# Optimization experiments

Measured on AMD Instinct MI355X. Metric: run time of the kernel, lower is better.

The kernel has to match this reference:

```python
import jax, jax.numpy as jnp
import numpy as np

N_NODES = 100000
N_EDGES = 1000000
DIM = 64
BN_EPS = 1e-5


def setup_inputs() -> dict:
    key = jax.random.key(0)
    k_x, k_src, k_off, k_w, k_b = jax.random.split(key, 5)
    x = jax.random.normal(k_x, (N_NODES, DIM), dtype=jnp.float32)
    # Build edges with src != dst so add_remaining_self_loops semantics reduce to
    # appending one self-loop per node (no pre-existing self loops).
    src = jax.random.randint(k_src, (N_EDGES,), 0, N_NODES, dtype=jnp.int64)
    off = jax.random.randint(k_off, (N_EDGES,), 1, N_NODES, dtype=jnp.int64)
    dst = (src + off) % N_NODES
    edge_index = jnp.stack([src, dst], axis=0)
    lin_w = jax.random.normal(k_w, (DIM, DIM), dtype=jnp.float32) * (1.0 / np.sqrt(DIM))
    lin_b = jax.random.normal(k_b, (DIM,), dtype=jnp.float32) * 0.01
    bn_gamma = jnp.ones((DIM,), dtype=jnp.float32)
    bn_beta = jnp.zeros((DIM,), dtype=jnp.float32)
    return {"x": x, "edge_index": edge_index, "lin_w": lin_w, "lin_b": lin_b,
            "bn_gamma": bn_gamma, "bn_beta": bn_beta}


def reference(x, edge_index, lin_w, lin_b, bn_gamma, bn_beta):
    N = x.shape[0]
    loops = jnp.arange(N, dtype=edge_index.dtype)
    src = jnp.concatenate([edge_index[0], loops])  # add_remaining_self_loops
    dst = jnp.concatenate([edge_index[1], loops])
    # edge_weight is rebound to None inside MySAGEConv.forward, so message == x_j
    msgs = jnp.take(x, src, axis=0)                      # [E+N, D] gather
    summed = jax.ops.segment_sum(msgs, dst, num_segments=N)
    deg = jax.ops.segment_sum(jnp.ones_like(dst, dtype=x.dtype), dst, num_segments=N)
    aggr = summed / deg[:, None]                         # scatter-mean (deg >= 1)
    out = aggr @ lin_w.T + lin_b                         # linear
    # BatchNorm1d, training mode (batch stats, biased variance)
    mean = out.mean(axis=0)
    var = out.var(axis=0)
    out = (out - mean) * jax.lax.rsqrt(var + BN_EPS) * bn_gamma + bn_beta
    out = out + x                                        # residual (in_dim == out_dim)
    return jax.nn.relu(out)
```

## Files before the change

kernel.cpp:

```cpp
#include <hip/hip_runtime.h>

#define N_NODES 100000
#define N_EDGES 1000000
#define DIM 64
#define BN_EPS 1e-5f

#define CAP 40
#define NSEG 100
#define SEG_NODES 1000
#define SEGCAP 11264
#define BCAP 64
#define EPB 3072
#define NBIN1 326
#define CONV_BLOCKS 3125
#define OVF_CAP 1024
#define GATHER_BLOCKS (N_NODES / 32)

typedef __attribute__((ext_vector_type(8))) short short8_t;
typedef __attribute__((ext_vector_type(4))) float f32x4;

__device__ inline unsigned bf16rne(float f) {
    unsigned u = __float_as_uint(f);
    return (u + 0x7FFFu + ((u >> 16) & 1u)) >> 16;
}
__device__ inline unsigned pack2(float a, float b) {
    return bf16rne(a) | (bf16rne(b) << 16);
}
__device__ inline void unp_add(unsigned d, float& e0, float& e1) {
    e0 += __uint_as_float(d << 16);
    e1 += __uint_as_float(d & 0xFFFF0000u);
}
__device__ inline void add8(float* acc, uint4 v) {
    unp_add(v.x, acc[0], acc[1]);
    unp_add(v.y, acc[2], acc[3]);
    unp_add(v.z, acc[4], acc[5]);
    unp_add(v.w, acc[6], acc[7]);
}

__global__ __launch_bounds__(256) void k_bin1(const int* __restrict__ ei,
                                              const float4* __restrict__ x4,
                                              const float* __restrict__ W,
                                              uint2* __restrict__ seg_buf,
                                              int* __restrict__ seg_cnt,
                                              int* __restrict__ ovf_cnt,
                                              uint2* __restrict__ ovf,
                                              uint4* __restrict__ xh,
                                              unsigned short* __restrict__ Wb) {
    __shared__ int cnt[NSEG];
    __shared__ int base[NSEG];
    __shared__ uint2 pairs[NSEG][BCAP];

    int b = blockIdx.x;
    if (b == NBIN1 + CONV_BLOCKS) {
        for (int t = threadIdx.x; t < DIM * DIM / 2; t += 256) {
            float2 w2 = ((const float2*)W)[t];
            ((unsigned*)Wb)[t] = pack2(w2.x, w2.y);
        }
        return;
    }
    if (b >= NBIN1) {
        int g = (b - NBIN1) * 256 + threadIdx.x;
        float4 lo = x4[2 * g];
        float4 hi = x4[2 * g + 1];
        uint4 r;
        r.x = pack2(lo.x, lo.y);
        r.y = pack2(lo.z, lo.w);
        r.z = pack2(hi.x, hi.y);
        r.w = pack2(hi.z, hi.w);
        xh[8 + g] = r;
        return;
    }

    for (int t = threadIdx.x; t < NSEG; t += 256) cnt[t] = 0;
    __syncthreads();

    const int base4 = b * (EPB / 4);
#pragma unroll
    for (int k = 0; k < 3; ++k) {
        int i4 = base4 + k * 256 + threadIdx.x;
        if (i4 < N_EDGES / 4) {
            int4 s4 = ((const int4*)ei)[i4];
            int4 d4 = ((const int4*)(ei + N_EDGES))[i4];
            int ss[4] = {s4.x, s4.y, s4.z, s4.w};
            int dd[4] = {d4.x, d4.y, d4.z, d4.w};
#pragma unroll
            for (int q = 0; q < 4; ++q) {
                int seg = (unsigned)dd[q] / SEG_NODES;
                int p = atomicAdd(&cnt[seg], 1);
                if (p < BCAP) {
                    pairs[seg][p] = make_uint2((unsigned)ss[q], (unsigned)dd[q]);
                } else {
                    int g = atomicAdd(ovf_cnt, 1);
                    if (g < OVF_CAP) ovf[g] = make_uint2((unsigned)ss[q], (unsigned)dd[q]);
                }
            }
        }
    }
    __syncthreads();

    if (threadIdx.x < NSEG) {
        int c = min(cnt[threadIdx.x], BCAP);
        base[threadIdx.x] = atomicAdd(&seg_cnt[threadIdx.x], c);
    }
    __syncthreads();

    const int wave = threadIdx.x >> 6, lane = threadIdx.x & 63;
    for (int seg = wave; seg < NSEG; seg += 4) {
        int c = min(cnt[seg], BCAP);
        int bs = base[seg];
        for (int i = lane; i < c; i += 64) {
            int pos = bs + i;
            if (pos < SEGCAP) seg_buf[seg * SEGCAP + pos] = pairs[seg][i];
        }
    }
}

__global__ __launch_bounds__(256) void k_bin2(const uint2* __restrict__ seg_buf,
                                              const int* __restrict__ seg_cnt,
                                              const int* __restrict__ ovf_cnt,
                                              const uint2* __restrict__ ovf,
                                              int* __restrict__ srcs,
                                              int* __restrict__ count) {
    const int s = blockIdx.x;
    __shared__ int lcnt[SEG_NODES];
    for (int t = threadIdx.x; t < SEG_NODES; t += 256) lcnt[t] = 0;
    __syncthreads();

    int n = seg_cnt[s];
    if (n > SEGCAP) n = SEGCAP;
    const uint2* sb = seg_buf + s * SEGCAP;

    auto place = [&](uint2 pr) {
        int dl = (int)pr.y - s * SEG_NODES;
        int p = atomicAdd(&lcnt[dl], 1);
        if (p < CAP) srcs[(int)pr.y * CAP + p] = (int)pr.x;
    };

    int i = threadIdx.x;
    for (; i + 768 < n; i += 1024) {
        uint2 a0 = sb[i];
        uint2 a1 = sb[i + 256];
        uint2 a2 = sb[i + 512];
        uint2 a3 = sb[i + 768];
        place(a0); place(a1); place(a2); place(a3);
    }
    for (; i < n; i += 256) place(sb[i]);

    int oc = *ovf_cnt;
    if (oc > OVF_CAP) oc = OVF_CAP;
    for (int t = threadIdx.x; t < oc; t += 256) {
        uint2 pr = ovf[t];
        if ((int)((unsigned)pr.y / SEG_NODES) == s) place(pr);
    }
    __syncthreads();

    for (int t = threadIdx.x; t < SEG_NODES; t += 256)
        count[s * SEG_NODES + t] = lcnt[t];
}

__global__ __launch_bounds__(256) void k_fill_legacy(const int* __restrict__ ei,
                                                     const float4* __restrict__ x4,
                                                     const float* __restrict__ W,
                                                     int* __restrict__ count,
                                                     int* __restrict__ srcs,
                                                     uint4* __restrict__ xh,
                                                     unsigned short* __restrict__ Wb) {
    int b = blockIdx.x;
    if (b == 977 + CONV_BLOCKS) {
        for (int t = threadIdx.x; t < DIM * DIM / 2; t += 256) {
            float2 w2 = ((const float2*)W)[t];
            ((unsigned*)Wb)[t] = pack2(w2.x, w2.y);
        }
        return;
    }
    if (b < 977) {
        int t = b * 256 + threadIdx.x;
        if (t < N_EDGES / 4) {
            int4 s4 = ((const int4*)ei)[t];
            int4 d4 = ((const int4*)(ei + N_EDGES))[t];
            int p0 = atomicAdd(&count[d4.x], 1);
            int p1 = atomicAdd(&count[d4.y], 1);
            int p2 = atomicAdd(&count[d4.z], 1);
            int p3 = atomicAdd(&count[d4.w], 1);
            if (p0 < CAP) srcs[d4.x * CAP + p0] = s4.x;
            if (p1 < CAP) srcs[d4.y * CAP + p1] = s4.y;
            if (p2 < CAP) srcs[d4.z * CAP + p2] = s4.z;
            if (p3 < CAP) srcs[d4.w * CAP + p3] = s4.w;
        }
    } else {
        int g = (b - 977) * 256 + threadIdx.x;
        float4 lo = x4[2 * g];
        float4 hi = x4[2 * g + 1];
        uint4 r;
        r.x = pack2(lo.x, lo.y);
        r.y = pack2(lo.z, lo.w);
        r.z = pack2(hi.x, hi.y);
        r.w = pack2(hi.z, hi.w);
        xh[8 + g] = r;
    }
}

__global__ __launch_bounds__(256) void k_gather_linear(
        const uint4* __restrict__ xh,
        const int* __restrict__ count,
        const int* __restrict__ srcs,
        const unsigned short* __restrict__ Wb,
        const float* __restrict__ bias,
        float* __restrict__ lin_out,
        float* __restrict__ stats8) {
    const int lane = threadIdx.x & 63;
    const int wave = threadIdx.x >> 6;
    const int sub  = lane >> 3;
    const int f8   = lane & 7;

    __shared__ unsigned short ab[32 * 72];
    __shared__ float red0[4][32], red1[4][32];

    const int row = blockIdx.x * 32 + wave * 8 + sub;
    float acc[8] = {0.f, 0.f, 0.f, 0.f, 0.f, 0.f, 0.f, 0.f};
    add8(acc, xh[(row + 1) * 8 + f8]);

    const int ctrue = count[row];
    const int c = (ctrue < CAP) ? ctrue : CAP;
    const int* sp = srcs + row * CAP;
    for (int i = 0; i < c; i += 4) {
        int4 e = *(const int4*)(sp + i);
        int e1 = (i + 1 < c) ? e.y : -1;
        int e2 = (i + 2 < c) ? e.z : -1;
        int e3 = (i + 3 < c) ? e.w : -1;
        uint4 v0 = xh[(e.x + 1) * 8 + f8];
        uint4 v1 = xh[(e1 + 1) * 8 + f8];
        uint4 v2 = xh[(e2 + 1) * 8 + f8];
        uint4 v3 = xh[(e3 + 1) * 8 + f8];
        add8(acc, v0);
        add8(acc, v1);
        add8(acc, v2);
        add8(acc, v3);
    }

    const float inv = 1.0f / (float)(ctrue + 1);
#pragma unroll
    for (int k = 0; k < 8; ++k) acc[k] *= inv;

    uint4 pk;
    pk.x = pack2(acc[0], acc[1]);
    pk.y = pack2(acc[2], acc[3]);
    pk.z = pack2(acc[4], acc[5]);
    pk.w = pack2(acc[6], acc[7]);
    *(uint4*)&ab[(wave * 8 + sub) * 72 + f8 * 8] = pk;
    __syncthreads();

    const int mh = wave & 1, nh = wave >> 1;
    const int m = lane & 15, quad = lane >> 4;

    const unsigned short* ap = &ab[(mh * 16 + m) * 72 + quad * 8];
    short8_t a0 = *(const short8_t*)ap;
    short8_t a1 = *(const short8_t*)(ap + 32);

    const unsigned short* bp0 = Wb + (nh * 32 + m) * 64 + quad * 8;
    short8_t b00 = *(const short8_t*)bp0;
    short8_t b01 = *(const short8_t*)(bp0 + 32);
    const unsigned short* bp1 = bp0 + 16 * 64;
    short8_t b10 = *(const short8_t*)bp1;
    short8_t b11 = *(const short8_t*)(bp1 + 32);

    f32x4 c0 = {0.f, 0.f, 0.f, 0.f}, c1 = {0.f, 0.f, 0.f, 0.f};
    c0 = __builtin_amdgcn_mfma_f32_16x16x32_bf16(a0, b00, c0, 0, 0, 0);
    c0 = __builtin_amdgcn_mfma_f32_16x16x32_bf16(a1, b01, c0, 0, 0, 0);
    c1 = __builtin_amdgcn_mfma_f32_16x16x32_bf16(a0, b10, c1, 0, 0, 0);
    c1 = __builtin_amdgcn_mfma_f32_16x16x32_bf16(a1, b11, c1, 0, 0, 0);

    const int rb = blockIdx.x * 32 + mh * 16 + quad * 4;
#pragma unroll
    for (int f = 0; f < 2; ++f) {
        f32x4 cc = f ? c1 : c0;
        int col = nh * 32 + f * 16 + m;
        float bj = bias[col];
        float q0 = 0.f, q1 = 0.f;
#pragma unroll
        for (int r = 0; r < 4; ++r) {
            float v = cc[r] + bj;
            lin_out[(rb + r) * DIM + col] = v;
            q0 += v;
            q1 += v * v;
        }
        q0 += __shfl_xor(q0, 16); q0 += __shfl_xor(q0, 32);
        q1 += __shfl_xor(q1, 16); q1 += __shfl_xor(q1, 32);
        if (quad == 0) {
            red0[wave][f * 16 + m] = q0;
            red1[wave][f * 16 + m] = q1;
        }
    }
    __syncthreads();
    if (threadIdx.x < DIM) {
        int j = threadIdx.x, jh = j >> 5, jl = j & 31;
        float t0 = red0[2 * jh][jl] + red0[2 * jh + 1][jl];
        float t1 = red1[2 * jh][jl] + red1[2 * jh + 1][jl];
        float* sb = stats8 + (blockIdx.x & 7) * 128;
        atomicAdd(&sb[j], t0);
        atomicAdd(&sb[DIM + j], t1);
    }
}

__global__ __launch_bounds__(256) void k_final(const float4* lin4,
                                               const float4* __restrict__ x4,
                                               const float* __restrict__ stats8,
                                               const float* __restrict__ gamma,
                                               const float* __restrict__ beta,
                                               float4* out4) {
    __shared__ float ss[2][DIM];
    if (threadIdx.x < DIM) {
        int j = threadIdx.x;
        float s0 = 0.f, s1 = 0.f;
#pragma unroll
        for (int b = 0; b < 8; ++b) {
            s0 += stats8[b * 128 + j];
            s1 += stats8[b * 128 + DIM + j];
        }
        const float invN = 1.0f / (float)N_NODES;
        float mean = s0 * invN;
        float var = s1 * invN - mean * mean;
        float scale = gamma[j] * rsqrtf(var + BN_EPS);
        ss[0][j] = scale;
        ss[1][j] = beta[j] - mean * scale;
    }
    __syncthreads();
    int tid = blockIdx.x * blockDim.x + threadIdx.x;
    int j4 = (tid & (DIM / 4 - 1)) * 4;
    float4 l = lin4[tid];
    float4 xv = x4[tid];
    float4 o;
    o.x = fmaxf(fmaf(l.x, ss[0][j4 + 0], ss[1][j4 + 0]) + xv.x, 0.f);
    o.y = fmaxf(fmaf(l.y, ss[0][j4 + 1], ss[1][j4 + 1]) + xv.y, 0.f);
    o.z = fmaxf(fmaf(l.z, ss[0][j4 + 2], ss[1][j4 + 2]) + xv.z, 0.f);
    o.w = fmaxf(fmaf(l.w, ss[0][j4 + 3], ss[1][j4 + 3]) + xv.w, 0.f);
    out4[tid] = o;
}

extern "C" void kernel_launch(void* const* d_in, const int* in_sizes, int n_in,
                              void* d_out, int out_size, void* d_ws, size_t ws_size,
                              hipStream_t stream) {
    const float* x     = (const float*)d_in[0];
    const int*   ei    = (const int*)d_in[1];
    const float* W     = (const float*)d_in[2];
    const float* bias  = (const float*)d_in[3];
    const float* gamma = (const float*)d_in[4];
    const float* beta  = (const float*)d_in[5];
    float* out = (float*)d_out;

    char* ws = (char*)d_ws;
    float*          stats8  = (float*)(ws);
    int*            seg_cnt = (int*)(ws + 4096);
    int*            ovf_cnt = (int*)(ws + 4608);
    uint2*          ovf     = (uint2*)(ws + 4736);
    uint4*          xh      = (uint4*)(ws + 12928);
    unsigned short* Wb      = (unsigned short*)(ws + 12813056);
    int*            count   = (int*)(ws + 12821248);
    int*            srcs    = (int*)(ws + 13221248);
    uint2*          seg_buf = (uint2*)(ws + 29221248);

    const size_t NEED_BIN = 29221248 + (size_t)NSEG * SEGCAP * 8;

    if (ws_size >= NEED_BIN) {
        hipMemsetAsync(ws, 0, 13056, stream);
        k_bin1<<<NBIN1 + CONV_BLOCKS + 1, 256, 0, stream>>>(
            ei, (const float4*)x, W, seg_buf, seg_cnt, ovf_cnt, ovf, xh, Wb);
        k_bin2<<<NSEG, 256, 0, stream>>>(seg_buf, seg_cnt, ovf_cnt, ovf,
                                         srcs, count);
    } else {
        hipMemsetAsync(ws, 0, 13056, stream);
        hipMemsetAsync(count, 0, 400000, stream);
        k_fill_legacy<<<977 + CONV_BLOCKS + 1, 256, 0, stream>>>(
            ei, (const float4*)x, W, count, srcs, xh, Wb);
    }

    k_gather_linear<<<GATHER_BLOCKS, 256, 0, stream>>>(
        xh, count, srcs, Wb, bias, out, stats8);

    k_final<<<N_NODES * (DIM / 4) / 256, 256, 0, stream>>>(
        (const float4*)out, (const float4*)x, stats8, gamma, beta, (float4*)out);
}
```

Measured before the change: 153.6 us.

## Fuse all stages into one persistent kernel with grid barriers

Replaces the separate binning, placement, gather-linear and BatchNorm-finalize kernels with a single persistent kernel. Stages are separated by software grid-wide barriers built on atomics. Linear outputs are held in registers across the BatchNorm-statistics barrier instead of being written to and re-read from global memory. The placement pass splits each segment into four sub-blocks, and the residual reads the bf16 copy of x. This aims to cut launch overhead and the global round-trip, but it relies on all blocks being co-resident for the barriers, adds register pressure, and changes the residual precision.

```diff
diff --git a/kernel.cpp b/kernel.cpp
--- a/kernel.cpp
+++ b/kernel.cpp
@@ -8,13 +8,17 @@
 #define CAP 40
 #define NSEG 100
 #define SEG_NODES 1000
-#define SEGCAP 11264
-#define BCAP 64
+#define SEGCAP 11200
+#define BCAP 48
 #define EPB 3072
 #define NBIN1 326
-#define CONV_BLOCKS 3125
-#define OVF_CAP 1024
-#define GATHER_BLOCKS (N_NODES / 32)
+#define CONV_CHUNKS 3125
+#define TOTAL_P1 (NBIN1 + CONV_CHUNKS + 1)
+#define OVF_CAP 4096
+#define SPLITB 4
+#define SEG_Q (SEG_NODES / SPLITB)
+#define NTILES (N_NODES / 32)
+#define MAXT 5
 
 typedef __attribute__((ext_vector_type(8))) short short8_t;
 typedef __attribute__((ext_vector_type(4))) float f32x4;
@@ -37,225 +41,136 @@
     unp_add(v.w, acc[6], acc[7]);
 }
 
-__global__ __launch_bounds__(256) void k_bin1(const int* __restrict__ ei,
-                                              const float4* __restrict__ x4,
-                                              const float* __restrict__ W,
-                                              uint2* __restrict__ seg_buf,
-                                              int* __restrict__ seg_cnt,
-                                              int* __restrict__ ovf_cnt,
-                                              uint2* __restrict__ ovf,
-                                              uint4* __restrict__ xh,
-                                              unsigned short* __restrict__ Wb) {
-    __shared__ int cnt[NSEG];
-    __shared__ int base[NSEG];
-    __shared__ uint2 pairs[NSEG][BCAP];
-
-    int b = blockIdx.x;
-    if (b == NBIN1 + CONV_BLOCKS) {
-        for (int t = threadIdx.x; t < DIM * DIM / 2; t += 256) {
-            float2 w2 = ((const float2*)W)[t];
-            ((unsigned*)Wb)[t] = pack2(w2.x, w2.y);
-        }
-        return;
-    }
-    if (b >= NBIN1) {
-        int g = (b - NBIN1) * 256 + threadIdx.x;
-        float4 lo = x4[2 * g];
-        float4 hi = x4[2 * g + 1];
-        uint4 r;
-        r.x = pack2(lo.x, lo.y);
-        r.y = pack2(lo.z, lo.w);
-        r.z = pack2(hi.x, hi.y);
-        r.w = pack2(hi.z, hi.w);
-        xh[8 + g] = r;
-        return;
-    }
-
-    for (int t = threadIdx.x; t < NSEG; t += 256) cnt[t] = 0;
+__device__ inline void gbar(int* bar, int nblk) {
     __syncthreads();
-
-    const int base4 = b * (EPB / 4);
-#pragma unroll
-    for (int k = 0; k < 3; ++k) {
-        int i4 = base4 + k * 256 + threadIdx.x;
-        if (i4 < N_EDGES / 4) {
-            int4 s4 = ((const int4*)ei)[i4];
-            int4 d4 = ((const int4*)(ei + N_EDGES))[i4];
-            int ss[4] = {s4.x, s4.y, s4.z, s4.w};
-            int dd[4] = {d4.x, d4.y, d4.z, d4.w};
-#pragma unroll
-            for (int q = 0; q < 4; ++q) {
-                int seg = (unsigned)dd[q] / SEG_NODES;
-                int p = atomicAdd(&cnt[seg], 1);
-                if (p < BCAP) {
-                    pairs[seg][p] = make_uint2((unsigned)ss[q], (unsigned)dd[q]);
-                } else {
-                    int g = atomicAdd(ovf_cnt, 1);
-                    if (g < OVF_CAP) ovf[g] = make_uint2((unsigned)ss[q], (unsigned)dd[q]);
-                }
-            }
-        }
+    if (threadIdx.x == 0) {
+        __hip_atomic_fetch_add(bar, 1, __ATOMIC_ACQ_REL, __HIP_MEMORY_SCOPE_AGENT);
+        while (__hip_atomic_load(bar, __ATOMIC_ACQUIRE, __HIP_MEMORY_SCOPE_AGENT) < nblk)
+            __builtin_amdgcn_s_sleep(2);
     }
     __syncthreads();
-
-    if (threadIdx.x < NSEG) {
-        int c = min(cnt[threadIdx.x], BCAP);
-        base[threadIdx.x] = atomicAdd(&seg_cnt[threadIdx.x], c);
-    }
-    __syncthreads();
-
-    const int wave = threadIdx.x >> 6, lane = threadIdx.x & 63;
-    for (int seg = wave; seg < NSEG; seg += 4) {
-        int c = min(cnt[seg], BCAP);
-        int bs = base[seg];
-        for (int i = lane; i < c; i += 64) {
-            int pos = bs + i;
-            if (pos < SEGCAP) seg_buf[seg * SEGCAP + pos] = pairs[seg][i];
-        }
-    }
-}
-
-__global__ __launch_bounds__(256) void k_bin2(const uint2* __restrict__ seg_buf,
-                                              const int* __restrict__ seg_cnt,
-                                              const int* __restrict__ ovf_cnt,
-                                              const uint2* __restrict__ ovf,
-                                              int* __restrict__ srcs,
-                                              int* __restrict__ count) {
-    const int s = blockIdx.x;
-    __shared__ int lcnt[SEG_NODES];
-    for (int t = threadIdx.x; t < SEG_NODES; t += 256) lcnt[t] = 0;
-    __syncthreads();
-
-    int n = seg_cnt[s];
-    if (n > SEGCAP) n = SEGCAP;
-    const uint2* sb = seg_buf + s * SEGCAP;
-
-    auto place = [&](uint2 pr) {
-        int dl = (int)pr.y - s * SEG_NODES;
-        int p = atomicAdd(&lcnt[dl], 1);
-        if (p < CAP) srcs[(int)pr.y * CAP + p] = (int)pr.x;
-    };
-
-    int i = threadIdx.x;
-    for (; i + 768 < n; i += 1024) {
-        uint2 a0 = sb[i];
-        uint2 a1 = sb[i + 256];
-        uint2 a2 = sb[i + 512];
-        uint2 a3 = sb[i + 768];
-        place(a0); place(a1); place(a2); place(a3);
-    }
-    for (; i < n; i += 256) place(sb[i]);
-
-    int oc = *ovf_cnt;
-    if (oc > OVF_CAP) oc = OVF_CAP;
-    for (int t = threadIdx.x; t < oc; t += 256) {
-        uint2 pr = ovf[t];
-        if ((int)((unsigned)pr.y / SEG_NODES) == s) place(pr);
-    }
-    __syncthreads();
-
-    for (int t = threadIdx.x; t < SEG_NODES; t += 256)
-        count[s * SEG_NODES + t] = lcnt[t];
-}
-
-__global__ __launch_bounds__(256) void k_fill_legacy(const int* __restrict__ ei,
-                                                     const float4* __restrict__ x4,
-                                                     const float* __restrict__ W,
-                                                     int* __restrict__ count,
-                                                     int* __restrict__ srcs,
-                                                     uint4* __restrict__ xh,
-                                                     unsigned short* __restrict__ Wb) {
-    int b = blockIdx.x;
-    if (b == 977 + CONV_BLOCKS) {
-        for (int t = threadIdx.x; t < DIM * DIM / 2; t += 256) {
-            float2 w2 = ((const float2*)W)[t];
-            ((unsigned*)Wb)[t] = pack2(w2.x, w2.y);
-        }
-        return;
-    }
-    if (b < 977) {
-        int t = b * 256 + threadIdx.x;
-        if (t < N_EDGES / 4) {
-            int4 s4 = ((const int4*)ei)[t];
-            int4 d4 = ((const int4*)(ei + N_EDGES))[t];
-            int p0 = atomicAdd(&count[d4.x], 1);
-            int p1 = atomicAdd(&count[d4.y], 1);
-            int p2 = atomicAdd(&count[d4.z], 1);
-            int p3 = atomicAdd(&count[d4.w], 1);
-            if (p0 < CAP) srcs[d4.x * CAP + p0] = s4.x;
-            if (p1 < CAP) srcs[d4.y * CAP + p1] = s4.y;
-            if (p2 < CAP) srcs[d4.z * CAP + p2] = s4.z;
-            if (p3 < CAP) srcs[d4.w * CAP + p3] = s4.w;
-        }
-    } else {
-        int g = (b - 977) * 256 + threadIdx.x;
-        float4 lo = x4[2 * g];
-        float4 hi = x4[2 * g + 1];
-        uint4 r;
-        r.x = pack2(lo.x, lo.y);
-        r.y = pack2(lo.z, lo.w);
-        r.z = pack2(hi.x, hi.y);
-        r.w = pack2(hi.z, hi.w);
-        xh[8 + g] = r;
-    }
-}
-
-__global__ __launch_bounds__(256) void k_gather_linear(
-        const uint4* __restrict__ xh,
-        const int* __restrict__ count,
-        const int* __restrict__ srcs,
-        const unsigned short* __restrict__ Wb,
-        const float* __restrict__ bias,
-        float* __restrict__ lin_out,
-        float* __restrict__ stats8) {
+}
+
+union SharedU {
+    struct { int cnt[NSEG]; int base[NSEG]; uint2 pairs[NSEG][BCAP]; } p1;
+    struct { int lcnt[SEG_Q]; } p2;
+    struct { unsigned short ab[32 * 72]; float red0[4][32]; float red1[4][32]; } p3;
+    struct { float ss[2][DIM]; } p4;
+};
+
+__global__ __launch_bounds__(256) void k_mega(
+        const int* __restrict__ ei, const float4* __restrict__ x4,
+        const float* __restrict__ W, const float* __restrict__ bias,
+        const float* __restrict__ gamma, const float* __restrict__ beta,
+        float* __restrict__ out,
+        int* __restrict__ seg_cnt, int* __restrict__ ovf_cnt,
+        int* __restrict__ bar, uint2* __restrict__ ovf,
+        uint4* __restrict__ xh, unsigned short* __restrict__ Wb,
+        int* __restrict__ count, int* __restrict__ srcs,
+        uint2* __restrict__ seg_buf, float* __restrict__ stats8,
+        int nblk) {
+    __shared__ SharedU sh;
     const int lane = threadIdx.x & 63;
     const int wave = threadIdx.x >> 6;
-    const int sub  = lane >> 3;
-    const int f8   = lane & 7;
-
-    __shared__ unsigned short ab[32 * 72];
-    __shared__ float red0[4][32], red1[4][32];
-
-    const int row = blockIdx.x * 32 + wave * 8 + sub;
-    float acc[8] = {0.f, 0.f, 0.f, 0.f, 0.f, 0.f, 0.f, 0.f};
-    add8(acc, xh[(row + 1) * 8 + f8]);
-
-    const int ctrue = count[row];
-    const int c = (ctrue < CAP) ? ctrue : CAP;
-    const int* sp = srcs + row * CAP;
-    for (int i = 0; i < c; i += 4) {
-        int4 e = *(const int4*)(sp + i);
-        int e1 = (i + 1 < c) ? e.y : -1;
-        int e2 = (i + 2 < c) ? e.z : -1;
-        int e3 = (i + 3 < c) ? e.w : -1;
-        uint4 v0 = xh[(e.x + 1) * 8 + f8];
-        uint4 v1 = xh[(e1 + 1) * 8 + f8];
-        uint4 v2 = xh[(e2 + 1) * 8 + f8];
-        uint4 v3 = xh[(e3 + 1) * 8 + f8];
-        add8(acc, v0);
-        add8(acc, v1);
-        add8(acc, v2);
-        add8(acc, v3);
-    }
-
-    const float inv = 1.0f / (float)(ctrue + 1);
-#pragma unroll
-    for (int k = 0; k < 8; ++k) acc[k] *= inv;
-
-    uint4 pk;
-    pk.x = pack2(acc[0], acc[1]);
-    pk.y = pack2(acc[2], acc[3]);
-    pk.z = pack2(acc[4], acc[5]);
-    pk.w = pack2(acc[6], acc[7]);
-    *(uint4*)&ab[(wave * 8 + sub) * 72 + f8 * 8] = pk;
-    __syncthreads();
-
+
+    for (int vb = blockIdx.x; vb < TOTAL_P1; vb += gridDim.x) {
+        if (vb == NBIN1 + CONV_CHUNKS) {
+            for (int t = threadIdx.x; t < DIM * DIM / 2; t += 256) {
+                float2 w2 = ((const float2*)W)[t];
+                ((unsigned*)Wb)[t] = pack2(w2.x, w2.y);
+            }
+            continue;
+        }
+        if (vb >= NBIN1) {
+            int g = (vb - NBIN1) * 256 + threadIdx.x;
+            float4 lo = x4[2 * g];
+            float4 hi = x4[2 * g + 1];
+            uint4 r;
+            r.x = pack2(lo.x, lo.y);
+            r.y = pack2(lo.z, lo.w);
+            r.z = pack2(hi.x, hi.y);
+            r.w = pack2(hi.z, hi.w);
+            xh[8 + g] = r;
+            continue;
+        }
+        __syncthreads();
+        for (int t = threadIdx.x; t < NSEG; t += 256) sh.p1.cnt[t] = 0;
+        __syncthreads();
+        const int base4 = vb * (EPB / 4);
+#pragma unroll
+        for (int kk = 0; kk < 3; ++kk) {
+            int i4 = base4 + kk * 256 + threadIdx.x;
+            if (i4 < N_EDGES / 4) {
+                int4 s4 = ((const int4*)ei)[i4];
+                int4 d4 = ((const int4*)(ei + N_EDGES))[i4];
+                int ssx[4] = {s4.x, s4.y, s4.z, s4.w};
+                int ddx[4] = {d4.x, d4.y, d4.z, d4.w};
+#pragma unroll
+                for (int q = 0; q < 4; ++q) {
+                    int seg = (unsigned)ddx[q] / SEG_NODES;
+                    int p = atomicAdd(&sh.p1.cnt[seg], 1);
+                    if (p < BCAP) {
+                        sh.p1.pairs[seg][p] = make_uint2((unsigned)ssx[q], (unsigned)ddx[q]);
+                    } else {
+                        int g = atomicAdd(ovf_cnt, 1);
+                        if (g < OVF_CAP) ovf[g] = make_uint2((unsigned)ssx[q], (unsigned)ddx[q]);
+                    }
+                }
+            }
+        }
+        __syncthreads();
+        if (threadIdx.x < NSEG) {
+            int c = min(sh.p1.cnt[threadIdx.x], BCAP);
+            sh.p1.base[threadIdx.x] = atomicAdd(&seg_cnt[threadIdx.x], c);
+        }
+        __syncthreads();
+        for (int seg = wave; seg < NSEG; seg += 4) {
+            int c = min(sh.p1.cnt[seg], BCAP);
+            int bs = sh.p1.base[seg];
+            for (int i = lane; i < c; i += 64) {
+                int pos = bs + i;
+                if (pos < SEGCAP) seg_buf[seg * SEGCAP + pos] = sh.p1.pairs[seg][i];
+            }
+        }
+    }
+    gbar(&bar[0], nblk);
+
+    for (int vb = blockIdx.x; vb < NSEG * SPLITB; vb += gridDim.x) {
+        const int s = vb >> 2, q = vb & 3;
+        __syncthreads();
+        for (int t = threadIdx.x; t < SEG_Q; t += 256) sh.p2.lcnt[t] = 0;
+        __syncthreads();
+        int n = seg_cnt[s];
+        if (n > SEGCAP) n = SEGCAP;
+        const uint2* sb = seg_buf + s * SEGCAP;
+        const int lo = q * SEG_Q, hi = lo + SEG_Q;
+        for (int i = threadIdx.x; i < n; i += 256) {
+            uint2 pr = sb[i];
+            int dl = (int)pr.y - s * SEG_NODES;
+            if (dl >= lo && dl < hi) {
+                int p = atomicAdd(&sh.p2.lcnt[dl - lo], 1);
+                if (p < CAP) srcs[(int)pr.y * CAP + p] = (int)pr.x;
+            }
+        }
+        int oc = *ovf_cnt;
+        if (oc > OVF_CAP) oc = OVF_CAP;
+        for (int t = threadIdx.x; t < oc; t += 256) {
+            uint2 pr = ovf[t];
+            int dl = (int)pr.y - s * SEG_NODES;
+            if (dl >= lo && dl < hi) {
+                int p = atomicAdd(&sh.p2.lcnt[dl - lo], 1);
+                if (p < CAP) srcs[(int)pr.y * CAP + p] = (int)pr.x;
+            }
+        }
+        __syncthreads();
+        for (int t = threadIdx.x; t < SEG_Q; t += 256)
+            count[s * SEG_NODES + lo + t] = sh.p2.lcnt[t];
+    }
+    gbar(&bar[1], nblk);
+
+    const int sub = lane >> 3, f8 = lane & 7;
     const int mh = wave & 1, nh = wave >> 1;
     const int m = lane & 15, quad = lane >> 4;
-
-    const unsigned short* ap = &ab[(mh * 16 + m) * 72 + quad * 8];
-    short8_t a0 = *(const short8_t*)ap;
-    short8_t a1 = *(const short8_t*)(ap + 32);
 
     const unsigned short* bp0 = Wb + (nh * 32 + m) * 64 + quad * 8;
     short8_t b00 = *(const short8_t*)bp0;
@@ -263,52 +178,93 @@
     const unsigned short* bp1 = bp0 + 16 * 64;
     short8_t b10 = *(const short8_t*)bp1;
     short8_t b11 = *(const short8_t*)(bp1 + 32);
-
-    f32x4 c0 = {0.f, 0.f, 0.f, 0.f}, c1 = {0.f, 0.f, 0.f, 0.f};
-    c0 = __builtin_amdgcn_mfma_f32_16x16x32_bf16(a0, b00, c0, 0, 0, 0);
-    c0 = __builtin_amdgcn_mfma_f32_16x16x32_bf16(a1, b01, c0, 0, 0, 0);
-    c1 = __builtin_amdgcn_mfma_f32_16x16x32_bf16(a0, b10, c1, 0, 0, 0);
-    c1 = __builtin_amdgcn_mfma_f32_16x16x32_bf16(a1, b11, c1, 0, 0, 0);
-
-    const int rb = blockIdx.x * 32 + mh * 16 + quad * 4;
-#pragma unroll
-    for (int f = 0; f < 2; ++f) {
-        f32x4 cc = f ? c1 : c0;
-        int col = nh * 32 + f * 16 + m;
-        float bj = bias[col];
-        float q0 = 0.f, q1 = 0.f;
-#pragma unroll
-        for (int r = 0; r < 4; ++r) {
-            float v = cc[r] + bj;
-            lin_out[(rb + r) * DIM + col] = v;
-            q0 += v;
-            q1 += v * v;
-        }
-        q0 += __shfl_xor(q0, 16); q0 += __shfl_xor(q0, 32);
-        q1 += __shfl_xor(q1, 16); q1 += __shfl_xor(q1, 32);
-        if (quad == 0) {
-            red0[wave][f * 16 + m] = q0;
-            red1[wave][f * 16 + m] = q1;
-        }
-    }
-    __syncthreads();
-    if (threadIdx.x < DIM) {
-        int j = threadIdx.x, jh = j >> 5, jl = j & 31;
-        float t0 = red0[2 * jh][jl] + red0[2 * jh + 1][jl];
-        float t1 = red1[2 * jh][jl] + red1[2 * jh + 1][jl];
-        float* sb = stats8 + (blockIdx.x & 7) * 128;
-        atomicAdd(&sb[j], t0);
-        atomicAdd(&sb[DIM + j], t1);
-    }
-}
-
-__global__ __launch_bounds__(256) void k_final(const float4* lin4,
-                                               const float4* __restrict__ x4,
-                                               const float* __restrict__ stats8,
-                                               const float* __restrict__ gamma,
-                                               const float* __restrict__ beta,
-                                               float4* out4) {
-    __shared__ float ss[2][DIM];
+    const float bj0 = bias[nh * 32 + m];
+    const float bj1 = bias[nh * 32 + 16 + m];
+
+    f32x4 cst[MAXT][2];
+    int k = 0;
+    for (int tile = blockIdx.x; tile < NTILES; tile += gridDim.x, ++k) {
+        const int row = tile * 32 + wave * 8 + sub;
+        float acc[8] = {0.f, 0.f, 0.f, 0.f, 0.f, 0.f, 0.f, 0.f};
+        add8(acc, xh[(row + 1) * 8 + f8]);
+        const int ctrue = count[row];
+        const int c = (ctrue < CAP) ? ctrue : CAP;
+        const int* sp = srcs + row * CAP;
+        for (int i = 0; i < c; i += 4) {
+            int4 e = *(const int4*)(sp + i);
+            int e1 = (i + 1 < c) ? e.y : -1;
+            int e2 = (i + 2 < c) ? e.z : -1;
+            int e3 = (i + 3 < c) ? e.w : -1;
+            uint4 v0 = xh[(e.x + 1) * 8 + f8];
+            uint4 v1 = xh[(e1 + 1) * 8 + f8];
+            uint4 v2 = xh[(e2 + 1) * 8 + f8];
+            uint4 v3 = xh[(e3 + 1) * 8 + f8];
+            add8(acc, v0);
+            add8(acc, v1);
+            add8(acc, v2);
+            add8(acc, v3);
+        }
+        const float inv = 1.0f / (float)(ctrue + 1);
+#pragma unroll
+        for (int j = 0; j < 8; ++j) acc[j] *= inv;
+
+        __syncthreads();
+        uint4 pk;
+        pk.x = pack2(acc[0], acc[1]);
+        pk.y = pack2(acc[2], acc[3]);
+        pk.z = pack2(acc[4], acc[5]);
+        pk.w = pack2(acc[6], acc[7]);
+        *(uint4*)&sh.p3.ab[(wave * 8 + sub) * 72 + f8 * 8] = pk;
+        __syncthreads();
+
+        const unsigned short* ap = &sh.p3.ab[(mh * 16 + m) * 72 + quad * 8];
+        short8_t a0 = *(const short8_t*)ap;
+        short8_t a1 = *(const short8_t*)(ap + 32);
+
+        f32x4 c0 = {0.f, 0.f, 0.f, 0.f}, c1 = {0.f, 0.f, 0.f, 0.f};
+        c0 = __builtin_amdgcn_mfma_f32_16x16x32_bf16(a0, b00, c0, 0, 0, 0);
+        c0 = __builtin_amdgcn_mfma_f32_16x16x32_bf16(a1, b01, c0, 0, 0, 0);
+        c1 = __builtin_amdgcn_mfma_f32_16x16x32_bf16(a0, b10, c1, 0, 0, 0);
+        c1 = __builtin_amdgcn_mfma_f32_16x16x32_bf16(a1, b11, c1, 0, 0, 0);
+
+        const int rb = tile * 32 + mh * 16 + quad * 4;
+#pragma unroll
+        for (int f = 0; f < 2; ++f) {
+            f32x4 cc = f ? c1 : c0;
+            float bj = f ? bj1 : bj0;
+            float q0 = 0.f, q1 = 0.f;
+#pragma unroll
+            for (int r = 0; r < 4; ++r) {
+                float v = cc[r] + bj;
+                cc[r] = v;
+                q0 += v;
+                q1 += v * v;
+            }
+            if (k < MAXT) cst[k][f] = cc;
+            else {
+                int col = nh * 32 + f * 16 + m;
+#pragma unroll
+                for (int r = 0; r < 4; ++r) out[(rb + r) * DIM + col] = cc[r];
+            }
+            q0 += __shfl_xor(q0, 16); q0 += __shfl_xor(q0, 32);
+            q1 += __shfl_xor(q1, 16); q1 += __shfl_xor(q1, 32);
+            if (quad == 0) {
+                sh.p3.red0[wave][f * 16 + m] = q0;
+                sh.p3.red1[wave][f * 16 + m] = q1;
+            }
+        }
+        __syncthreads();
+        if (threadIdx.x < DIM) {
+            int j = threadIdx.x, jh = j >> 5, jl = j & 31;
+            float t0 = sh.p3.red0[2 * jh][jl] + sh.p3.red0[2 * jh + 1][jl];
+            float t1 = sh.p3.red1[2 * jh][jl] + sh.p3.red1[2 * jh + 1][jl];
+            float* sb = stats8 + (blockIdx.x & 7) * 128;
+            atomicAdd(&sb[j], t0);
+            atomicAdd(&sb[DIM + j], t1);
+        }
+    }
+    gbar(&bar[2], nblk);
+
     if (threadIdx.x < DIM) {
         int j = threadIdx.x;
         float s0 = 0.f, s1 = 0.f;
@@ -321,20 +277,29 @@
         float mean = s0 * invN;
         float var = s1 * invN - mean * mean;
         float scale = gamma[j] * rsqrtf(var + BN_EPS);
-        ss[0][j] = scale;
-        ss[1][j] = beta[j] - mean * scale;
+        sh.p4.ss[0][j] = scale;
+        sh.p4.ss[1][j] = beta[j] - mean * scale;
     }
     __syncthreads();
-    int tid = blockIdx.x * blockDim.x + threadIdx.x;
-    int j4 = (tid & (DIM / 4 - 1)) * 4;
-    float4 l = lin4[tid];
-    float4 xv = x4[tid];
-    float4 o;
-    o.x = fmaxf(fmaf(l.x, ss[0][j4 + 0], ss[1][j4 + 0]) + xv.x, 0.f);
-    o.y = fmaxf(fmaf(l.y, ss[0][j4 + 1], ss[1][j4 + 1]) + xv.y, 0.f);
-    o.z = fmaxf(fmaf(l.z, ss[0][j4 + 2], ss[1][j4 + 2]) + xv.z, 0.f);
-    o.w = fmaxf(fmaf(l.w, ss[0][j4 + 3], ss[1][j4 + 3]) + xv.w, 0.f);
-    out4[tid] = o;
+
+    const unsigned short* xh16 = (const unsigned short*)xh;
+    k = 0;
+    for (int tile = blockIdx.x; tile < NTILES; tile += gridDim.x, ++k) {
+        const int rb = tile * 32 + mh * 16 + quad * 4;
+#pragma unroll
+        for (int f = 0; f < 2; ++f) {
+            int col = nh * 32 + f * 16 + m;
+            float sc = sh.p4.ss[0][col];
+            float sf = sh.p4.ss[1][col];
+#pragma unroll
+            for (int r = 0; r < 4; ++r) {
+                float v = (k < MAXT) ? cst[k][f][r] : out[(rb + r) * DIM + col];
+                unsigned short h = xh16[(rb + r + 1) * 64 + col];
+                float xr = __uint_as_float((unsigned)h << 16);
+                out[(rb + r) * DIM + col] = fmaxf(fmaf(v, sc, sf) + xr, 0.f);
+            }
+        }
+    }
 }
 
 extern "C" void kernel_launch(void* const* d_in, const int* in_sizes, int n_in,
@@ -352,31 +317,28 @@
     float*          stats8  = (float*)(ws);
     int*            seg_cnt = (int*)(ws + 4096);
     int*            ovf_cnt = (int*)(ws + 4608);
+    int*            bar     = (int*)(ws + 4612);
     uint2*          ovf     = (uint2*)(ws + 4736);
-    uint4*          xh      = (uint4*)(ws + 12928);
-    unsigned short* Wb      = (unsigned short*)(ws + 12813056);
-    int*            count   = (int*)(ws + 12821248);
-    int*            srcs    = (int*)(ws + 13221248);
-    uint2*          seg_buf = (uint2*)(ws + 29221248);
-
-    const size_t NEED_BIN = 29221248 + (size_t)NSEG * SEGCAP * 8;
-
-    if (ws_size >= NEED_BIN) {
-        hipMemsetAsync(ws, 0, 13056, stream);
-        k_bin1<<<NBIN1 + CONV_BLOCKS + 1, 256, 0, stream>>>(
-            ei, (const float4*)x, W, seg_buf, seg_cnt, ovf_cnt, ovf, xh, Wb);
-        k_bin2<<<NSEG, 256, 0, stream>>>(seg_buf, seg_cnt, ovf_cnt, ovf,
-                                         srcs, count);
-    } else {
-        hipMemsetAsync(ws, 0, 13056, stream);
-        hipMemsetAsync(count, 0, 400000, stream);
-        k_fill_legacy<<<977 + CONV_BLOCKS + 1, 256, 0, stream>>>(
-            ei, (const float4*)x, W, count, srcs, xh, Wb);
-    }
-
-    k_gather_linear<<<GATHER_BLOCKS, 256, 0, stream>>>(
-        xh, count, srcs, Wb, bias, out, stats8);
-
-    k_final<<<N_NODES * (DIM / 4) / 256, 256, 0, stream>>>(
-        (const float4*)out, (const float4*)x, stats8, gamma, beta, (float4*)out);
-}
+    uint4*          xh      = (uint4*)(ws + 37504);
+    unsigned short* Wb      = (unsigned short*)(ws + 12837632);
+    int*            count   = (int*)(ws + 12845824);
+    int*            srcs    = (int*)(ws + 13245824);
+    uint2*          seg_buf = (uint2*)(ws + 29245824);
+
+    int ncu = 256;
+    hipDeviceGetAttribute(&ncu, hipDeviceAttributeMultiprocessorCount, 0);
+    int nb = 0;
+    if (hipOccupancyMaxActiveBlocksPerMultiprocessor(&nb, k_mega, 256, 0)
+            != hipSuccess || nb < 1)
+        nb = 2;
+    long nblk = (long)nb * ncu;
+    if (nblk > 2048) nblk = 2048;
+    if (nblk < 64) nblk = 64;
+
+    hipMemsetAsync(ws, 0, 37632, stream);
+
+    k_mega<<<(int)nblk, 256, 0, stream>>>(
+        ei, (const float4*)x, W, bias, gamma, beta, out,
+        seg_cnt, ovf_cnt, bar, ovf, xh, Wb, count, srcs, seg_buf, stats8,
+        (int)nblk);
+}
```

Result: slower. 413.3 us (+169.1%).
